# Performance work log

Hardware: AMD Instinct MI355X
Metric: run time of the kernel (lower is better)

Reference implementation:

```python
import jax, jax.numpy as jnp
import numpy as np

DECAY = 0.9  # module init_kwarg: decay


def setup_inputs() -> dict:
    key = jax.random.key(0)
    ks = jax.random.split(key, 5)
    T, B, I, H = 512, 256, 256, 1024
    return {
        "input": jax.random.normal(ks[0], (T, B, I), dtype=jnp.float32),
        "hidden_init": jax.random.normal(ks[1], (1, B, H), dtype=jnp.float32),
        "weight_ih": jax.random.normal(ks[2], (H, I), dtype=jnp.float32) * (1.0 / np.sqrt(I)),
        "weight_hh": jax.random.normal(ks[3], (H, H), dtype=jnp.float32) * (1.0 / np.sqrt(H)),
        "bias": jax.random.normal(ks[4], (H,), dtype=jnp.float32) * 0.01,
    }


def reference(input, hidden_init, weight_ih, weight_hh, bias):
    # input: [T, B, I] time-major; hidden_init: [1, B, H]
    h0 = hidden_init[0]
    alpha = 1.0 - DECAY

    def step(h, x_t):
        # x_t: [B, I]; h: [B, H]
        activity = jnp.tanh(x_t @ weight_ih.T + h @ weight_hh.T + bias)
        h_new = DECAY * h + alpha * activity
        return h_new, h_new

    h_last, outputs = jax.lax.scan(step, h0, input)
    return outputs, h_last  # outputs: [T, B, H]
```

## Files before the change

### kernel.cpp

```cpp
#include <hip/hip_runtime.h>
#include <hip/hip_bf16.h>
#include <math.h>

#define T_STEPS 512
#define B_SZ 256
#define I_SZ 256
#define H_SZ 1024

typedef unsigned short u16;
typedef __bf16 bf16x8 __attribute__((ext_vector_type(8)));
typedef float f32x4 __attribute__((ext_vector_type(4)));

__device__ __forceinline__ u16 f2bf(float f) {
    union { float f; unsigned u; } v; v.f = f;
    unsigned r = v.u + 0x7fffu + ((v.u >> 16) & 1u);
    return (u16)(r >> 16);
}

template<int OFF>
__device__ __forceinline__ bf16x8 ld_b128_sc(const u16* p) {
    bf16x8 r;
    asm volatile("global_load_dwordx4 %0, %1, off offset:%2 sc0 sc1"
                 : "=v"(r) : "v"(p), "i"(OFF));
    return r;
}

__device__ __forceinline__ void st_b16_sc(u16* p, unsigned v) {
    asm volatile("global_store_short %0, %1, off sc0 sc1"
                 :: "v"(p), "v"(v) : "memory");
}

__device__ __forceinline__ f32x4 mm(bf16x8 a, bf16x8 b, f32x4 c) {
    return __builtin_amdgcn_mfma_f32_16x16x32_bf16(a, b, c, 0, 0, 0);
}

#define WAITV(N) do { \
    asm volatile("s_waitcnt vmcnt(" #N ")" ::: "memory"); \
    __builtin_amdgcn_sched_barrier(0); \
} while (0)

#define LD_GRP(arr, B0) do { \
    arr[0] = ld_b128_sc<((B0)+0)*64>(hrow); \
    arr[1] = ld_b128_sc<((B0)+1)*64>(hrow); \
    arr[2] = ld_b128_sc<((B0)+2)*64>(hrow); \
    arr[3] = ld_b128_sc<((B0)+3)*64>(hrow); \
    arr[4] = ld_b128_sc<((B0)+4)*64>(hrow); \
    arr[5] = ld_b128_sc<((B0)+5)*64>(hrow); \
    arr[6] = ld_b128_sc<((B0)+6)*64>(hrow); \
    arr[7] = ld_b128_sc<((B0)+7)*64>(hrow); \
} while (0)

#define MM_GRP(arr, B0) do { \
    acc0 = mm(arr[0], wB[(B0)+0], acc0); \
    acc1 = mm(arr[1], wB[(B0)+1], acc1); \
    acc2 = mm(arr[2], wB[(B0)+2], acc2); \
    acc3 = mm(arr[3], wB[(B0)+3], acc3); \
    acc0 = mm(arr[4], wB[(B0)+4], acc0); \
    acc1 = mm(arr[5], wB[(B0)+5], acc1); \
    acc2 = mm(arr[6], wB[(B0)+6], acc2); \
    acc3 = mm(arr[7], wB[(B0)+7], acc3); \
} while (0)

__global__ void prep_kernel(const float* __restrict__ wih, const float* __restrict__ whh,
                            const float* __restrict__ h0,
                            u16* __restrict__ whh_b, u16* __restrict__ wih_b,
                            u16* __restrict__ hp0, unsigned* __restrict__ ctr) {
    int idx = blockIdx.x * blockDim.x + threadIdx.x;
    int stride = gridDim.x * blockDim.x;
    for (int i = idx; i < H_SZ * H_SZ; i += stride) whh_b[i] = f2bf(whh[i]);
    for (int i = idx; i < H_SZ * I_SZ; i += stride) wih_b[i] = f2bf(wih[i]);
    for (int i = idx; i < B_SZ * H_SZ; i += stride) hp0[i] = f2bf(h0[i]);
    if (idx < 8) ctr[idx] = 0;
}

__global__ void __launch_bounds__(256, 1)
rnn_persistent(const float* __restrict__ x, const float* __restrict__ h0,
               const float* __restrict__ bias,
               const u16* __restrict__ whh_b, const u16* __restrict__ wih_b,
               u16* __restrict__ hp0, u16* __restrict__ hp1,
               unsigned* __restrict__ ctr, float* __restrict__ out)
{
    const int tid  = threadIdx.x;
    const int wid  = tid >> 6;
    const int lane = tid & 63;
    const int l16  = lane & 15;
    const int quad = lane >> 4;

    const int team  = blockIdx.x & 7;
    const int slice = blockIdx.x >> 3;

    const int row_base = team * 32 + (wid & 1) * 16;
    const int gcol     = slice * 32 + (wid >> 1) * 16 + l16;
    const int am       = row_base + l16;
    const int kq       = quad * 8;

    bf16x8 wB[32];
#pragma unroll
    for (int kk = 0; kk < 32; ++kk)
        wB[kk] = *reinterpret_cast<const bf16x8*>(whh_b + gcol * H_SZ + kk * 32 + kq);
    bf16x8 wI[8];
#pragma unroll
    for (int kx = 0; kx < 8; ++kx)
        wI[kx] = *reinterpret_cast<const bf16x8*>(wih_b + gcol * I_SZ + kx * 32 + kq);

    const float bias_v = bias[gcol];

    float hown[4];
#pragma unroll
    for (int i = 0; i < 4; ++i)
        hown[i] = h0[(row_base + quad * 4 + i) * H_SZ + gcol];

    unsigned* my_ctr = ctr + team;

    for (int t = 0; t < T_STEPS; ++t) {
        const u16* hcur = (t & 1) ? hp1 : hp0;
        u16*       hnxt = (t & 1) ? hp0 : hp1;

        f32x4 acc0 = {0.f,0.f,0.f,0.f}, acc1 = {0.f,0.f,0.f,0.f};
        f32x4 acc2 = {0.f,0.f,0.f,0.f}, acc3 = {0.f,0.f,0.f,0.f};

        const float* xrow = x + (size_t)t * (B_SZ * I_SZ) + am * I_SZ + kq;
#pragma unroll
        for (int kx = 0; kx < 8; ++kx) {
            f32x4 x0 = *reinterpret_cast<const f32x4*>(xrow + kx * 32);
            f32x4 x1 = *reinterpret_cast<const f32x4*>(xrow + kx * 32 + 4);
            union { u16 u[8]; bf16x8 v; } ax;
#pragma unroll
            for (int j = 0; j < 4; ++j) { ax.u[j] = f2bf(x0[j]); ax.u[4 + j] = f2bf(x1[j]); }
            if ((kx & 3) == 0)      acc0 = mm(ax.v, wI[kx], acc0);
            else if ((kx & 3) == 1) acc1 = mm(ax.v, wI[kx], acc1);
            else if ((kx & 3) == 2) acc2 = mm(ax.v, wI[kx], acc2);
            else                    acc3 = mm(ax.v, wI[kx], acc3);
        }

        if (t > 0) {
            if (tid == 0) {
                const unsigned tgt = 32u * (unsigned)t;
                while (__hip_atomic_load(my_ctr, __ATOMIC_RELAXED, __HIP_MEMORY_SCOPE_AGENT) < tgt)
                    __builtin_amdgcn_s_sleep(1);
            }
            __syncthreads();
        }

        const u16* hrow = hcur + am * H_SZ + kq;
        bf16x8 g0[8], g1[8], g2[8], g3[8];
        LD_GRP(g0, 0);
        LD_GRP(g1, 8);
        WAITV(8);
        MM_GRP(g0, 0);
        LD_GRP(g2, 16);
        WAITV(8);
        MM_GRP(g1, 8);
        LD_GRP(g3, 24);
        WAITV(8);
        MM_GRP(g2, 16);
        WAITV(0);
        MM_GRP(g3, 24);

        float hn[4];
#pragma unroll
        for (int i = 0; i < 4; ++i) {
            float pre = (acc0[i] + acc1[i]) + (acc2[i] + acc3[i]) + bias_v;
            hn[i] = 0.9f * hown[i] + 0.1f * tanhf(pre);
            hown[i] = hn[i];
        }

#pragma unroll
        for (int i = 0; i < 4; ++i)
            st_b16_sc(hnxt + (row_base + quad * 4 + i) * H_SZ + gcol,
                      (unsigned)f2bf(hn[i]));

        asm volatile("s_waitcnt vmcnt(0)" ::: "memory");
        __syncthreads();
        if (tid == 0)
            __hip_atomic_fetch_add(my_ctr, 1u, __ATOMIC_RELAXED, __HIP_MEMORY_SCOPE_AGENT);

        float* orow = out + (size_t)t * (B_SZ * H_SZ);
#pragma unroll
        for (int i = 0; i < 4; ++i)
            orow[(row_base + quad * 4 + i) * H_SZ + gcol] = hn[i];

        if (t == T_STEPS - 1) {
            float* hl = out + (size_t)T_STEPS * (B_SZ * H_SZ);
#pragma unroll
            for (int i = 0; i < 4; ++i)
                hl[(row_base + quad * 4 + i) * H_SZ + gcol] = hn[i];
        }
    }
}

extern "C" void kernel_launch(void* const* d_in, const int* in_sizes, int n_in,
                              void* d_out, int out_size, void* d_ws, size_t ws_size,
                              hipStream_t stream) {
    const float* x    = (const float*)d_in[0];
    const float* h0   = (const float*)d_in[1];
    const float* wih  = (const float*)d_in[2];
    const float* whh  = (const float*)d_in[3];
    const float* bias = (const float*)d_in[4];
    float* out = (float*)d_out;

    char* ws = (char*)d_ws;
    u16* whh_b = (u16*)(ws);
    u16* wih_b = (u16*)(ws + (size_t)(2u << 20));
    u16* hp0   = (u16*)(ws + (size_t)(2u << 20) + (1u << 19));
    u16* hp1   = (u16*)(ws + (size_t)(2u << 20) + (2u << 19));
    unsigned* ctr = (unsigned*)(ws + (size_t)(2u << 20) + (3u << 19));

    prep_kernel<<<dim3(1024), dim3(256), 0, stream>>>(wih, whh, h0, whh_b, wih_b, hp0, ctr);
    rnn_persistent<<<dim3(256), dim3(256), 0, stream>>>(x, h0, bias, whh_b, wih_b, hp0, hp1, ctr, out);
}
```

Baseline: 5.471 ms.

## Replace atomic team counter with per-wave step flags and prefetch next input

Each wave now publishes its own step-number flag with a plain coherent store after its hidden-state stores complete, and every wave polls all 128 team flags (two per lane) with a ballot. This replaces the block-wide syncthreads plus single-thread atomic add and sleep-polling. The next timestep's x rows are prefetched into registers at the end of each step, and all 32 hidden-state loads are issued before the input MFMAs with staged waits. The aim is to shorten the critical-path barrier latency between timesteps, at the cost of extra polling traffic and higher register pressure.

Measured after the change: 5.920 ms. +8.2%, slower.

```diff
diff --git a/kernel.cpp b/kernel.cpp
--- a/kernel.cpp
+++ b/kernel.cpp
@@ -8,6 +8,8 @@
 #define H_SZ 1024
 
 typedef unsigned short u16;
+typedef unsigned int u32;
+typedef unsigned long long u64;
 typedef __bf16 bf16x8 __attribute__((ext_vector_type(8)));
 typedef float f32x4 __attribute__((ext_vector_type(4)));
 
@@ -28,6 +30,18 @@
 __device__ __forceinline__ void st_b16_sc(u16* p, unsigned v) {
     asm volatile("global_store_short %0, %1, off sc0 sc1"
                  :: "v"(p), "v"(v) : "memory");
+}
+
+__device__ __forceinline__ void st_flag(u32* p, u32 v) {
+    asm volatile("global_store_dword %0, %1, off sc0 sc1"
+                 :: "v"(p), "v"(v) : "memory");
+}
+
+__device__ __forceinline__ u64 ld_flags2(const u32* p) {
+    u64 r;
+    asm volatile("global_load_dwordx2 %0, %1, off sc0 sc1"
+                 : "=v"(r) : "v"(p));
+    return r;
 }
 
 __device__ __forceinline__ f32x4 mm(bf16x8 a, bf16x8 b, f32x4 c) {
@@ -64,13 +78,13 @@
 __global__ void prep_kernel(const float* __restrict__ wih, const float* __restrict__ whh,
                             const float* __restrict__ h0,
                             u16* __restrict__ whh_b, u16* __restrict__ wih_b,
-                            u16* __restrict__ hp0, unsigned* __restrict__ ctr) {
+                            u16* __restrict__ hp0, u32* __restrict__ flags) {
     int idx = blockIdx.x * blockDim.x + threadIdx.x;
     int stride = gridDim.x * blockDim.x;
     for (int i = idx; i < H_SZ * H_SZ; i += stride) whh_b[i] = f2bf(whh[i]);
     for (int i = idx; i < H_SZ * I_SZ; i += stride) wih_b[i] = f2bf(wih[i]);
     for (int i = idx; i < B_SZ * H_SZ; i += stride) hp0[i] = f2bf(h0[i]);
-    if (idx < 8) ctr[idx] = 0;
+    if (idx < 8 * 32 * 4) flags[idx] = 0;
 }
 
 __global__ void __launch_bounds__(256, 1)
@@ -78,7 +92,7 @@
                const float* __restrict__ bias,
                const u16* __restrict__ whh_b, const u16* __restrict__ wih_b,
                u16* __restrict__ hp0, u16* __restrict__ hp1,
-               unsigned* __restrict__ ctr, float* __restrict__ out)
+               u32* __restrict__ flags, float* __restrict__ out)
 {
     const int tid  = threadIdx.x;
     const int wid  = tid >> 6;
@@ -110,52 +124,68 @@
     for (int i = 0; i < 4; ++i)
         hown[i] = h0[(row_base + quad * 4 + i) * H_SZ + gcol];
 
-    unsigned* my_ctr = ctr + team;
+    const u32* fl_poll = flags + team * 128 + lane * 2;
+    u32*       fl_mine = flags + team * 128 + slice * 4 + wid;
+
+    f32x4 xr[16];
+    {
+        const float* x0row = x + am * I_SZ + kq;
+#pragma unroll
+        for (int kx = 0; kx < 8; ++kx) {
+            xr[2 * kx]     = *reinterpret_cast<const f32x4*>(x0row + kx * 32);
+            xr[2 * kx + 1] = *reinterpret_cast<const f32x4*>(x0row + kx * 32 + 4);
+        }
+    }
 
     for (int t = 0; t < T_STEPS; ++t) {
         const u16* hcur = (t & 1) ? hp1 : hp0;
         u16*       hnxt = (t & 1) ? hp0 : hp1;
 
-        f32x4 acc0 = {0.f,0.f,0.f,0.f}, acc1 = {0.f,0.f,0.f,0.f};
-        f32x4 acc2 = {0.f,0.f,0.f,0.f}, acc3 = {0.f,0.f,0.f,0.f};
-
-        const float* xrow = x + (size_t)t * (B_SZ * I_SZ) + am * I_SZ + kq;
+        if (t > 0) {
+            const u32 tgt = (u32)t;
+            for (;;) {
+                u64 fv = ld_flags2(fl_poll);
+                asm volatile("s_waitcnt vmcnt(0)" : "+v"(fv) :: "memory");
+                __builtin_amdgcn_sched_barrier(0);
+                bool ok = ((u32)fv >= tgt) && ((u32)(fv >> 32) >= tgt);
+                if (__ballot(ok) == ~0ull) break;
+            }
+            __builtin_amdgcn_sched_barrier(0);
+        }
+
+        bf16x8 ax[8];
 #pragma unroll
         for (int kx = 0; kx < 8; ++kx) {
-            f32x4 x0 = *reinterpret_cast<const f32x4*>(xrow + kx * 32);
-            f32x4 x1 = *reinterpret_cast<const f32x4*>(xrow + kx * 32 + 4);
-            union { u16 u[8]; bf16x8 v; } ax;
-#pragma unroll
-            for (int j = 0; j < 4; ++j) { ax.u[j] = f2bf(x0[j]); ax.u[4 + j] = f2bf(x1[j]); }
-            if ((kx & 3) == 0)      acc0 = mm(ax.v, wI[kx], acc0);
-            else if ((kx & 3) == 1) acc1 = mm(ax.v, wI[kx], acc1);
-            else if ((kx & 3) == 2) acc2 = mm(ax.v, wI[kx], acc2);
-            else                    acc3 = mm(ax.v, wI[kx], acc3);
-        }
-
-        if (t > 0) {
-            if (tid == 0) {
-                const unsigned tgt = 32u * (unsigned)t;
-                while (__hip_atomic_load(my_ctr, __ATOMIC_RELAXED, __HIP_MEMORY_SCOPE_AGENT) < tgt)
-                    __builtin_amdgcn_s_sleep(1);
+            union { u16 u[8]; bf16x8 v; } c;
+#pragma unroll
+            for (int j = 0; j < 4; ++j) {
+                c.u[j]     = f2bf(xr[2 * kx][j]);
+                c.u[4 + j] = f2bf(xr[2 * kx + 1][j]);
             }
-            __syncthreads();
+            ax[kx] = c.v;
         }
 
         const u16* hrow = hcur + am * H_SZ + kq;
         bf16x8 g0[8], g1[8], g2[8], g3[8];
         LD_GRP(g0, 0);
         LD_GRP(g1, 8);
-        WAITV(8);
-        MM_GRP(g0, 0);
         LD_GRP(g2, 16);
-        WAITV(8);
-        MM_GRP(g1, 8);
         LD_GRP(g3, 24);
-        WAITV(8);
-        MM_GRP(g2, 16);
-        WAITV(0);
-        MM_GRP(g3, 24);
+
+        f32x4 acc0 = {0.f,0.f,0.f,0.f}, acc1 = {0.f,0.f,0.f,0.f};
+        f32x4 acc2 = {0.f,0.f,0.f,0.f}, acc3 = {0.f,0.f,0.f,0.f};
+#pragma unroll
+        for (int kx = 0; kx < 8; ++kx) {
+            if ((kx & 3) == 0)      acc0 = mm(ax[kx], wI[kx], acc0);
+            else if ((kx & 3) == 1) acc1 = mm(ax[kx], wI[kx], acc1);
+            else if ((kx & 3) == 2) acc2 = mm(ax[kx], wI[kx], acc2);
+            else                    acc3 = mm(ax[kx], wI[kx], acc3);
+        }
+
+        WAITV(24); MM_GRP(g0, 0);
+        WAITV(16); MM_GRP(g1, 8);
+        WAITV(8);  MM_GRP(g2, 16);
+        WAITV(0);  MM_GRP(g3, 24);
 
         float hn[4];
 #pragma unroll
@@ -169,11 +199,9 @@
         for (int i = 0; i < 4; ++i)
             st_b16_sc(hnxt + (row_base + quad * 4 + i) * H_SZ + gcol,
                       (unsigned)f2bf(hn[i]));
-
         asm volatile("s_waitcnt vmcnt(0)" ::: "memory");
-        __syncthreads();
-        if (tid == 0)
-            __hip_atomic_fetch_add(my_ctr, 1u, __ATOMIC_RELAXED, __HIP_MEMORY_SCOPE_AGENT);
+        __builtin_amdgcn_sched_barrier(0);
+        if (lane == 0) st_flag(fl_mine, (u32)(t + 1));
 
         float* orow = out + (size_t)t * (B_SZ * H_SZ);
 #pragma unroll
@@ -185,6 +213,15 @@
 #pragma unroll
             for (int i = 0; i < 4; ++i)
                 hl[(row_base + quad * 4 + i) * H_SZ + gcol] = hn[i];
+        }
+
+        if (t + 1 < T_STEPS) {
+            const float* xnrow = x + (size_t)(t + 1) * (B_SZ * I_SZ) + am * I_SZ + kq;
+#pragma unroll
+            for (int kx = 0; kx < 8; ++kx) {
+                xr[2 * kx]     = *reinterpret_cast<const f32x4*>(xnrow + kx * 32);
+                xr[2 * kx + 1] = *reinterpret_cast<const f32x4*>(xnrow + kx * 32 + 4);
+            }
         }
     }
 }
@@ -204,8 +241,8 @@
     u16* wih_b = (u16*)(ws + (size_t)(2u << 20));
     u16* hp0   = (u16*)(ws + (size_t)(2u << 20) + (1u << 19));
     u16* hp1   = (u16*)(ws + (size_t)(2u << 20) + (2u << 19));
-    unsigned* ctr = (unsigned*)(ws + (size_t)(2u << 20) + (3u << 19));
-
-    prep_kernel<<<dim3(1024), dim3(256), 0, stream>>>(wih, whh, h0, whh_b, wih_b, hp0, ctr);
-    rnn_persistent<<<dim3(256), dim3(256), 0, stream>>>(x, h0, bias, whh_b, wih_b, hp0, hp1, ctr, out);
-}
+    u32* flags = (u32*)(ws + (size_t)(2u << 20) + (3u << 19));
+
+    prep_kernel<<<dim3(1024), dim3(256), 0, stream>>>(wih, whh, h0, whh_b, wih_b, hp0, flags);
+    rnn_persistent<<<dim3(256), dim3(256), 0, stream>>>(x, h0, bias, whh_b, wih_b, hp0, hp1, flags, out);
+}
```
